# Optimization experiments

Measured on AMD Instinct MI355X. Metric: run time of the kernel, lower is better.

## Reference

```python
import jax, jax.numpy as jnp
import numpy as np

EPS = 1e-4  # Performer FAVOR+ stabilizing epsilon


def softmax_kernel(data, projection, is_query):
    # data: [b,h,s,d]; projection: [d,m] (already scaled by 1/sqrt(m) as in
    # redraw_projection_matrix). Performer softmax random-feature map:
    #   phi(x) = exp(x_hat @ P - ||x_hat||^2/2 - stabilizer) + eps
    d = data.shape[-1]
    data_normalizer = d ** -0.25
    data_dash = jnp.einsum('bhsd,dm->bhsm', data_normalizer * data, projection)
    diag = (jnp.sum(data * data, axis=-1, keepdims=True) * 0.5) * (data_normalizer ** 2)
    if is_query:
        stab = jnp.max(data_dash, axis=-1, keepdims=True)          # per-query max
    else:
        stab = jnp.max(data_dash, axis=(-2, -1), keepdims=True)    # per-head global max
    return jnp.exp(data_dash - diag - stab) + EPS


def setup_inputs() -> dict:
    key = jax.random.key(0)
    kq, kk, kv, kp = jax.random.split(key, 4)
    B, H, S, D, M = 4, 16, 1024, 64, 64
    q = jax.random.normal(kq, (B, H, S, D), dtype=jnp.float32)
    k = jax.random.normal(kk, (B, H, S, D), dtype=jnp.float32)
    v = jax.random.normal(kv, (B, H, S, D), dtype=jnp.float32)
    # simplex random matrix approximated by gaussian; scaled by 1/sqrt(n_features)
    projection_matrix = jax.random.normal(kp, (D, M), dtype=jnp.float32) / jnp.sqrt(jnp.float32(M))
    return {"q": q, "k": k, "v": v, "projection_matrix": projection_matrix}


def reference(q, k, v, projection_matrix):
    qp = softmax_kernel(q, projection_matrix, is_query=True)   # [b,h,s,m]
    kp = softmax_kernel(k, projection_matrix, is_query=False)  # [b,h,s,m]
    # torch impl: s = qp @ kp^T; causal tril; row-normalize; o = p @ v
    s = jnp.einsum('bhsm,bhtm->bhst', qp, kp)                  # [b,h,s,s]
    s = jnp.tril(s)
    p = s / jnp.sum(s, axis=-1, keepdims=True)
    return jnp.einsum('bhst,bhtd->bhsd', p, v)
```

## Files before the change

### kernel.cpp

```cpp
#include <hip/hip_runtime.h>
#include <hip/hip_bf16.h>


#define NRM 0.35355339059327373f
#define EPSF 1e-4f

typedef __attribute__((ext_vector_type(8))) short short8;
typedef __attribute__((ext_vector_type(4))) float f32x4;
typedef __attribute__((ext_vector_type(4))) unsigned uint4v;
typedef unsigned short u16;

__device__ inline u16 f2bf(float f) {
    unsigned u = __float_as_uint(f);
    return (u16)((u + 0x7FFFu + ((u >> 16) & 1u)) >> 16);
}
__device__ inline unsigned cvtpk(float lo, float hi) {
    unsigned r; asm("v_cvt_pk_bf16_f32 %0, %1, %2" : "=v"(r) : "v"(lo), "v"(hi)); return r;
}

__global__ __launch_bounds__(256) void kmax(
    const float* __restrict__ k, const float* __restrict__ proj,
    float* __restrict__ pmax, u16* __restrict__ ptg)
{
    __shared__ u16 PT[64][72];
    __shared__ float red[4];
    const int tid = threadIdx.x, lane = tid & 63, wave = tid >> 6;
    const int l15 = lane & 15, lhi = lane >> 4;
    const int b = blockIdx.x;

    #pragma unroll
    for (int p = 0; p < 4; ++p) {
        int d = p * 16 + (tid >> 4);
        int m = (tid & 15) * 4;
        float4 pv = *(const float4*)(proj + d * 64 + m);
        PT[m + 0][d] = f2bf(pv.x);
        PT[m + 1][d] = f2bf(pv.y);
        PT[m + 2][d] = f2bf(pv.z);
        PT[m + 3][d] = f2bf(pv.w);
    }
    __syncthreads();

    if (b == 0) {
        const int m = tid >> 2, c0 = (tid & 3) * 16;
        short8 x0 = *(const short8*)&PT[m][c0];
        short8 x1 = *(const short8*)&PT[m][c0 + 8];
        *(short8*)(ptg + m * 64 + c0)     = x0;
        *(short8*)(ptg + m * 64 + c0 + 8) = x1;
    }

    float m2 = -INFINITY;
    for (int i = 0; i < 4; ++i) {
        const int strip = b * 16 + wave * 4 + i;
        const int row0  = strip * 16;
        const float* xs = k + (size_t)(row0 + l15) * 64 + lhi * 8;
        float4 f0 = *(const float4*)(xs);
        float4 f1 = *(const float4*)(xs + 4);
        float4 f2 = *(const float4*)(xs + 32);
        float4 f3 = *(const float4*)(xs + 36);

        short8 a0, a1;
        a0[0] = (short)f2bf(f0.x); a0[1] = (short)f2bf(f0.y);
        a0[2] = (short)f2bf(f0.z); a0[3] = (short)f2bf(f0.w);
        a0[4] = (short)f2bf(f1.x); a0[5] = (short)f2bf(f1.y);
        a0[6] = (short)f2bf(f1.z); a0[7] = (short)f2bf(f1.w);
        a1[0] = (short)f2bf(f2.x); a1[1] = (short)f2bf(f2.y);
        a1[2] = (short)f2bf(f2.z); a1[3] = (short)f2bf(f2.w);
        a1[4] = (short)f2bf(f3.x); a1[5] = (short)f2bf(f3.y);
        a1[6] = (short)f2bf(f3.z); a1[7] = (short)f2bf(f3.w);

        f32x4 c[4] = { {0,0,0,0}, {0,0,0,0}, {0,0,0,0}, {0,0,0,0} };
        #pragma unroll
        for (int ct = 0; ct < 4; ++ct) {
            short8 b0 = *(const short8*)&PT[ct * 16 + l15][lhi * 8];
            short8 b1 = *(const short8*)&PT[ct * 16 + l15][32 + lhi * 8];
            c[ct] = __builtin_amdgcn_mfma_f32_16x16x32_bf16(a0, b0, c[ct], 0, 0, 0);
            c[ct] = __builtin_amdgcn_mfma_f32_16x16x32_bf16(a1, b1, c[ct], 0, 0, 0);
        }
        #pragma unroll
        for (int ct = 0; ct < 4; ++ct) {
            m2 = fmaxf(m2, fmaxf(fmaxf(c[ct][0], c[ct][1]), fmaxf(c[ct][2], c[ct][3])));
        }
    }
    m2 = fmaxf(m2, __shfl_xor(m2, 1));
    m2 = fmaxf(m2, __shfl_xor(m2, 2));
    m2 = fmaxf(m2, __shfl_xor(m2, 4));
    m2 = fmaxf(m2, __shfl_xor(m2, 8));
    m2 = fmaxf(m2, __shfl_xor(m2, 16));
    m2 = fmaxf(m2, __shfl_xor(m2, 32));
    if (lane == 0) red[wave] = m2 * NRM;
    __syncthreads();
    if (tid == 0)
        pmax[b] = fmaxf(fmaxf(red[0], red[1]), fmaxf(red[2], red[3]));
}

__global__ __launch_bounds__(256) void prep(
    const float* __restrict__ q, const float* __restrict__ k,
    const float* __restrict__ v, const u16* __restrict__ ptg,
    const float* __restrict__ pmax,
    u16* __restrict__ qp, u16* __restrict__ kp, u16* __restrict__ vT)
{
    __shared__ u16 tile[64][72];
    const int tid = threadIdx.x, lane = tid & 63, wave = tid >> 6;
    const int l15 = lane & 15, lhi = lane >> 4;
    const int bid = blockIdx.x;

    if (bid >= 512) {
        const int vb = bid - 512;
        for (int i = 0; i < 4; ++i) {
            const int t = vb * 4 + i;
            const int bh = t >> 4, s0 = (t & 15) << 6;
            const float* src = v + ((size_t)bh * 1024 + s0) * 64;
            #pragma unroll
            for (int p = 0; p < 4; ++p) {
                int s = p * 16 + (tid >> 4);
                int d = (tid & 15) * 4;
                float4 val = *(const float4*)(src + s * 64 + d);
                tile[d + 0][s] = f2bf(val.x);
                tile[d + 1][s] = f2bf(val.y);
                tile[d + 2][s] = f2bf(val.z);
                tile[d + 3][s] = f2bf(val.w);
            }
            __syncthreads();
            u16* dst = vT + (size_t)bh * 65536 + s0;
            #pragma unroll
            for (int p = 0; p < 4; ++p) {
                int d = p * 16 + (tid >> 4);
                int s = (tid & 15) * 4;
                ushort4 o;
                o.x = tile[d][s]; o.y = tile[d][s + 1];
                o.z = tile[d][s + 2]; o.w = tile[d][s + 3];
                *(ushort4*)(dst + d * 1024 + s) = o;
            }
            __syncthreads();
        }
        return;
    }

    const bool isQ = bid < 256;
    const float* x = isQ ? q : k;
    const int bid2 = bid & 255;

    short8 bf0[4], bf1[4];
    #pragma unroll
    for (int ct = 0; ct < 4; ++ct) {
        const u16* pr = ptg + (ct * 16 + l15) * 64 + lhi * 8;
        bf0[ct] = *(const short8*)(pr);
        bf1[ct] = *(const short8*)(pr + 32);
    }

    float stab = 0.f;
    if (!isQ) {
        const int h = bid2 >> 2;
        const float* pb = pmax + h * 4;
        stab = fmaxf(fmaxf(pb[0], pb[1]), fmaxf(pb[2], pb[3]));
    }

    for (int i = 0; i < 4; ++i) {
        const int strip = bid2 * 16 + wave * 4 + i;
        const int row0  = strip * 16;

        const float* xs = x + (size_t)(row0 + l15) * 64 + lhi * 8;
        float4 f0 = *(const float4*)(xs);
        float4 f1 = *(const float4*)(xs + 4);
        float4 f2 = *(const float4*)(xs + 32);
        float4 f3 = *(const float4*)(xs + 36);

        short8 a0, a1;
        a0[0] = (short)f2bf(f0.x); a0[1] = (short)f2bf(f0.y);
        a0[2] = (short)f2bf(f0.z); a0[3] = (short)f2bf(f0.w);
        a0[4] = (short)f2bf(f1.x); a0[5] = (short)f2bf(f1.y);
        a0[6] = (short)f2bf(f1.z); a0[7] = (short)f2bf(f1.w);
        a1[0] = (short)f2bf(f2.x); a1[1] = (short)f2bf(f2.y);
        a1[2] = (short)f2bf(f2.z); a1[3] = (short)f2bf(f2.w);
        a1[4] = (short)f2bf(f3.x); a1[5] = (short)f2bf(f3.y);
        a1[6] = (short)f2bf(f3.z); a1[7] = (short)f2bf(f3.w);

        float ss = f0.x*f0.x + f0.y*f0.y + f0.z*f0.z + f0.w*f0.w
                 + f1.x*f1.x + f1.y*f1.y + f1.z*f1.z + f1.w*f1.w
                 + f2.x*f2.x + f2.y*f2.y + f2.z*f2.z + f2.w*f2.w
                 + f3.x*f3.x + f3.y*f3.y + f3.z*f3.z + f3.w*f3.w;
        ss += __shfl_xor(ss, 16);
        ss += __shfl_xor(ss, 32);

        f32x4 c[4] = { {0,0,0,0}, {0,0,0,0}, {0,0,0,0}, {0,0,0,0} };
        #pragma unroll
        for (int ct = 0; ct < 4; ++ct) {
            c[ct] = __builtin_amdgcn_mfma_f32_16x16x32_bf16(a0, bf0[ct], c[ct], 0, 0, 0);
            c[ct] = __builtin_amdgcn_mfma_f32_16x16x32_bf16(a1, bf1[ct], c[ct], 0, 0, 0);
        }

        float diag[4];
        #pragma unroll
        for (int r = 0; r < 4; ++r) diag[r] = __shfl(ss, lhi * 4 + r) * 0.0625f;

        if (isQ) {
            float mx[4];
            #pragma unroll
            for (int r = 0; r < 4; ++r)
                mx[r] = fmaxf(fmaxf(c[0][r], c[1][r]), fmaxf(c[2][r], c[3][r]));
            #pragma unroll
            for (int r = 0; r < 4; ++r) {
                float m = mx[r];
                m = fmaxf(m, __shfl_xor(m, 1));
                m = fmaxf(m, __shfl_xor(m, 2));
                m = fmaxf(m, __shfl_xor(m, 4));
                m = fmaxf(m, __shfl_xor(m, 8));
                mx[r] = m;
            }
            u16* op = qp + (size_t)row0 * 64;
            #pragma unroll
            for (int ct = 0; ct < 4; ++ct) {
                #pragma unroll
                for (int r = 0; r < 4; ++r) {
                    float val = __expf(c[ct][r] * NRM - diag[r] - mx[r] * NRM) + EPSF;
                    op[(lhi * 4 + r) * 64 + ct * 16 + l15] = f2bf(val);
                }
            }
        } else {
            u16* op = kp + (size_t)row0 * 64;
            #pragma unroll
            for (int ct = 0; ct < 4; ++ct) {
                #pragma unroll
                for (int r = 0; r < 4; ++r) {
                    float val = __expf(c[ct][r] * NRM - diag[r] - stab) + EPSF;
                    op[(lhi * 4 + r) * 64 + ct * 16 + l15] = f2bf(val);
                }
            }
        }
    }
}

__global__ __launch_bounds__(256, 2) void attn(
    const u16* __restrict__ qp, const u16* __restrict__ kp,
    const u16* __restrict__ vT, float* __restrict__ out)
{
    __shared__ char lds[2][16384];

    const int tid = threadIdx.x, lane = tid & 63, wave = tid >> 6;
    const int l15 = lane & 15, lhi = lane >> 4;
    const int x = blockIdx.x;
    const int h = (((x >> 6) << 3)) | (x & 7);
    const int j = (x >> 3) & 7;

    const u16* kph = kp + (size_t)h * 65536;
    const u16* vTh = vT + (size_t)h * 65536;

    const int rch = lane >> 3;
    const int cb  = (lane & 7) * 16;
    const bool isK = wave < 2;
    const int cbase = (wave & 1) * 4;
    const int gstride = isK ? 4096 : 64;

    int lo0, lo1, lo2, lo3;
    const u16 *go0, *go1, *go2, *go3;
    {
        #define STG(cc, LO, GO)                                                 \
        {   int i = cbase + cc; int row = 8 * i + rch;                          \
            int nib = (row & 3) | (((row >> 3) & 1) << 2);                      \
            LO = (isK ? 0 : 8192) + row * 128 + (cb ^ (nib << 4));              \
            GO = isK ? (kph + row * 64 + (cb >> 1))                             \
                     : (vTh + (size_t)row * 1024 + (cb >> 1)); }
        STG(0, lo0, go0) STG(1, lo1, go1) STG(2, lo2, go2) STG(3, lo3, go3)
        #undef STG
    }

    const int rowp = 8 * (l15 >> 2) + (l15 & 3);
    const int nk = (l15 & 3) | (((l15 >> 2) & 1) << 2);
    const int nv = (l15 & 3) | (((l15 >> 3) & 1) << 2);
    const int ok0 = rowp * 128 + ((16 * lhi) ^ (nk << 4));
    const int ok1 = rowp * 128 + ((64 + 16 * lhi) ^ (nk << 4));
    const int ov0 = 8192 + l15 * 128 + ((16 * lhi) ^ (nv << 4));
    const int ov1 = 8192 + l15 * 128 + ((64 + 16 * lhi) ^ (nv << 4));

    short8 ls0, ls1, ls2, ls3;

    auto stageLoad = [&](int kt) {
        ls0 = *(const short8*)(go0 + (size_t)kt * gstride);
        ls1 = *(const short8*)(go1 + (size_t)kt * gstride);
        ls2 = *(const short8*)(go2 + (size_t)kt * gstride);
        ls3 = *(const short8*)(go3 + (size_t)kt * gstride);
    };
    auto stageWrite = [&](char* B) {
        *(short8*)(B + lo0) = ls0;
        *(short8*)(B + lo1) = ls1;
        *(short8*)(B + lo2) = ls2;
        *(short8*)(B + lo3) = ls3;
    };

    auto runStrip = [&](int sigma, int T) {
        const u16* qpr = qp + ((size_t)h * 1024 + sigma * 16 + l15) * 64 + lhi * 8;
        short8 aq0 = *(const short8*)(qpr);
        short8 aq1 = *(const short8*)(qpr + 32);
        const int qrl = ((sigma & 3) << 4) + l15;

        f32x4 acc0 = {0,0,0,0}, acc1 = {0,0,0,0}, acc2 = {0,0,0,0}, acc3 = {0,0,0,0};
        float den = 0.f;

        stageLoad(0);
        stageWrite(lds[0]);
        __syncthreads();

        int cur = 0;
        for (int kt = 0; kt <= T; ++kt) {
            if (kt < T) stageLoad(kt + 1);

            const char* B = lds[cur];
            short8 k0 = *(const short8*)(B + ok0);
            short8 k1 = *(const short8*)(B + ok1);
            short8 k2 = *(const short8*)(B + ok0 + 512);
            short8 k3 = *(const short8*)(B + ok1 + 512);
            short8 k4 = *(const short8*)(B + ok0 + 4096);
            short8 k5 = *(const short8*)(B + ok1 + 4096);
            short8 k6 = *(const short8*)(B + ok0 + 4608);
            short8 k7 = *(const short8*)(B + ok1 + 4608);
            short8 v0 = *(const short8*)(B + ov0);
            short8 v1 = *(const short8*)(B + ov1);
            short8 v2 = *(const short8*)(B + ov0 + 2048);
            short8 v3 = *(const short8*)(B + ov1 + 2048);
            short8 v4 = *(const short8*)(B + ov0 + 4096);
            short8 v5 = *(const short8*)(B + ov1 + 4096);
            short8 v6 = *(const short8*)(B + ov0 + 6144);
            short8 v7 = *(const short8*)(B + ov1 + 6144);

            f32x4 s0 = {0,0,0,0}, s1 = {0,0,0,0}, s2 = {0,0,0,0}, s3 = {0,0,0,0};
            __builtin_amdgcn_s_setprio(1);
            s0 = __builtin_amdgcn_mfma_f32_16x16x32_bf16(k0, aq0, s0, 0, 0, 0);
            s0 = __builtin_amdgcn_mfma_f32_16x16x32_bf16(k1, aq1, s0, 0, 0, 0);
            s1 = __builtin_amdgcn_mfma_f32_16x16x32_bf16(k2, aq0, s1, 0, 0, 0);
            s1 = __builtin_amdgcn_mfma_f32_16x16x32_bf16(k3, aq1, s1, 0, 0, 0);
            s2 = __builtin_amdgcn_mfma_f32_16x16x32_bf16(k4, aq0, s2, 0, 0, 0);
            s2 = __builtin_amdgcn_mfma_f32_16x16x32_bf16(k5, aq1, s2, 0, 0, 0);
            s3 = __builtin_amdgcn_mfma_f32_16x16x32_bf16(k6, aq0, s3, 0, 0, 0);
            s3 = __builtin_amdgcn_mfma_f32_16x16x32_bf16(k7, aq1, s3, 0, 0, 0);
            __builtin_amdgcn_s_setprio(0);

            if (kt == T) {
                const int kc = 8 * lhi;
                #pragma unroll
                for (int r = 0; r < 4; ++r) {
                    if (kc + r      > qrl) s0[r] = 0.f;
                    if (kc + 4 + r  > qrl) s1[r] = 0.f;
                    if (kc + 32 + r > qrl) s2[r] = 0.f;
                    if (kc + 36 + r > qrl) s3[r] = 0.f;
                }
            }
            float t0 = (s0[0] + s0[1]) + (s0[2] + s0[3]);
            float t1 = (s1[0] + s1[1]) + (s1[2] + s1[3]);
            float t2 = (s2[0] + s2[1]) + (s2[2] + s2[3]);
            float t3 = (s3[0] + s3[1]) + (s3[2] + s3[3]);
            den += (t0 + t1) + (t2 + t3);

            uint4v w0 = { cvtpk(s0[0], s0[1]), cvtpk(s0[2], s0[3]),
                          cvtpk(s1[0], s1[1]), cvtpk(s1[2], s1[3]) };
            uint4v w1 = { cvtpk(s2[0], s2[1]), cvtpk(s2[2], s2[3]),
                          cvtpk(s3[0], s3[1]), cvtpk(s3[2], s3[3]) };
            short8 pa0 = __builtin_bit_cast(short8, w0);
            short8 pa1 = __builtin_bit_cast(short8, w1);

            __builtin_amdgcn_s_setprio(1);
            acc0 = __builtin_amdgcn_mfma_f32_16x16x32_bf16(pa0, v0, acc0, 0, 0, 0);
            acc0 = __builtin_amdgcn_mfma_f32_16x16x32_bf16(pa1, v1, acc0, 0, 0, 0);
            acc1 = __builtin_amdgcn_mfma_f32_16x16x32_bf16(pa0, v2, acc1, 0, 0, 0);
            acc1 = __builtin_amdgcn_mfma_f32_16x16x32_bf16(pa1, v3, acc1, 0, 0, 0);
            acc2 = __builtin_amdgcn_mfma_f32_16x16x32_bf16(pa0, v4, acc2, 0, 0, 0);
            acc2 = __builtin_amdgcn_mfma_f32_16x16x32_bf16(pa1, v5, acc2, 0, 0, 0);
            acc3 = __builtin_amdgcn_mfma_f32_16x16x32_bf16(pa0, v6, acc3, 0, 0, 0);
            acc3 = __builtin_amdgcn_mfma_f32_16x16x32_bf16(pa1, v7, acc3, 0, 0, 0);
            __builtin_amdgcn_s_setprio(0);

            if (kt < T) stageWrite(lds[cur ^ 1]);
            __syncthreads();
            cur ^= 1;
        }

        den += __shfl_xor(den, 16);
        den += __shfl_xor(den, 32);
        float inv[4];
        #pragma unroll
        for (int r = 0; r < 4; ++r) inv[r] = 1.0f / __shfl(den, lhi * 4 + r);

        float* ob = out + ((size_t)h * 1024 + sigma * 16) * 64;
        #pragma unroll
        for (int r = 0; r < 4; ++r) {
            ob[(lhi * 4 + r) * 64 +  0 + l15] = acc0[r] * inv[r];
            ob[(lhi * 4 + r) * 64 + 16 + l15] = acc1[r] * inv[r];
            ob[(lhi * 4 + r) * 64 + 32 + l15] = acc2[r] * inv[r];
            ob[(lhi * 4 + r) * 64 + 48 + l15] = acc3[r] * inv[r];
        }
    };

    const int s0v = 4 * j + wave;
    runStrip(s0v, j);
    runStrip(63 - s0v, 15 - j);
}

extern "C" void kernel_launch(void* const* d_in, const int* in_sizes, int n_in,
                              void* d_out, int out_size, void* d_ws, size_t ws_size,
                              hipStream_t stream)
{
    const float* q    = (const float*)d_in[0];
    const float* k    = (const float*)d_in[1];
    const float* v    = (const float*)d_in[2];
    const float* proj = (const float*)d_in[3];
    float* out = (float*)d_out;

    char* ws = (char*)d_ws;
    u16*   qpw  = (u16*)(ws);
    u16*   kpw  = (u16*)(ws + (size_t)8 * 1024 * 1024);
    u16*   vTw  = (u16*)(ws + (size_t)16 * 1024 * 1024);
    float* pmax = (float*)(ws + (size_t)24 * 1024 * 1024);
    u16*   ptg  = (u16*)(ws + (size_t)24 * 1024 * 1024 + 4096);

    hipLaunchKernelGGL(kmax, dim3(256), dim3(256), 0, stream, k, proj, pmax, ptg);
    hipLaunchKernelGGL(prep, dim3(768), dim3(256), 0, stream,
                       q, k, v, ptg, pmax, qpw, kpw, vTw);
    hipLaunchKernelGGL(attn, dim3(512), dim3(256), 0, stream, qpw, kpw, vTw, out);
}
```

Before: 41.27 us.

## Fuse kmax, prep and attention into one cooperative kernel with grid syncs

Merges the three launches into a single cooperative kernel of 512 blocks. Each block computes its key strips' projections and keeps them in registers across a grid sync, so the key feature tensor is only written once after the global max is known and the key input is read once instead of twice. Query features and the V transpose are produced in the same phase, then a second grid sync precedes the causal attention loop. This removes launch gaps and redundant key loads, at the cost of two grid-wide barriers and a residency requirement of 2 blocks per CU. If the cooperative launch fails, it falls back to the old three-kernel path.

```diff
diff --git a/kernel.cpp b/kernel.cpp
--- a/kernel.cpp
+++ b/kernel.cpp
@@ -1,5 +1,8 @@
 #include <hip/hip_runtime.h>
 #include <hip/hip_bf16.h>
+#include <hip/hip_cooperative_groups.h>
+
+namespace cg = cooperative_groups;
 
 
 #define NRM 0.35355339059327373f
@@ -18,7 +21,375 @@
     unsigned r; asm("v_cvt_pk_bf16_f32 %0, %1, %2" : "=v"(r) : "v"(lo), "v"(hi)); return r;
 }
 
-__global__ __launch_bounds__(256) void kmax(
+__global__ __launch_bounds__(256, 2) void fused(
+    const float* __restrict__ q, const float* __restrict__ k,
+    const float* __restrict__ v, const float* __restrict__ proj,
+    float* __restrict__ pmax,
+    u16* __restrict__ qp, u16* __restrict__ kp, u16* __restrict__ vT,
+    float* __restrict__ out)
+{
+    __shared__ union {
+        struct { u16 PT[64][72]; u16 tile[64][72]; float red[4]; } p;
+        char attn[2][16384];
+    } smem;
+
+    const int tid = threadIdx.x, lane = tid & 63, wave = tid >> 6;
+    const int l15 = lane & 15, lhi = lane >> 4;
+    const int b = blockIdx.x;
+    cg::grid_group grid = cg::this_grid();
+
+    #pragma unroll
+    for (int p = 0; p < 4; ++p) {
+        int d = p * 16 + (tid >> 4);
+        int m = (tid & 15) * 4;
+        float4 pv = *(const float4*)(proj + d * 64 + m);
+        smem.p.PT[m + 0][d] = f2bf(pv.x);
+        smem.p.PT[m + 1][d] = f2bf(pv.y);
+        smem.p.PT[m + 2][d] = f2bf(pv.z);
+        smem.p.PT[m + 3][d] = f2bf(pv.w);
+    }
+    __syncthreads();
+
+    const int sA = b * 8 + wave * 2;
+    const int sB = sA + 1;
+
+    f32x4 cA[4] = {{0,0,0,0},{0,0,0,0},{0,0,0,0},{0,0,0,0}};
+    f32x4 cB[4] = {{0,0,0,0},{0,0,0,0},{0,0,0,0},{0,0,0,0}};
+    float diagA[4], diagB[4];
+    float m2 = -INFINITY;
+
+#define KSTRIP(SS, CC, DD)                                                      \
+    {                                                                           \
+        const int row0 = (SS) * 16;                                             \
+        const float* xs = k + (size_t)(row0 + l15) * 64 + lhi * 8;              \
+        float4 f0 = *(const float4*)(xs);                                       \
+        float4 f1 = *(const float4*)(xs + 4);                                   \
+        float4 f2 = *(const float4*)(xs + 32);                                  \
+        float4 f3 = *(const float4*)(xs + 36);                                  \
+        short8 a0, a1;                                                          \
+        a0[0]=(short)f2bf(f0.x); a0[1]=(short)f2bf(f0.y);                       \
+        a0[2]=(short)f2bf(f0.z); a0[3]=(short)f2bf(f0.w);                       \
+        a0[4]=(short)f2bf(f1.x); a0[5]=(short)f2bf(f1.y);                       \
+        a0[6]=(short)f2bf(f1.z); a0[7]=(short)f2bf(f1.w);                       \
+        a1[0]=(short)f2bf(f2.x); a1[1]=(short)f2bf(f2.y);                       \
+        a1[2]=(short)f2bf(f2.z); a1[3]=(short)f2bf(f2.w);                       \
+        a1[4]=(short)f2bf(f3.x); a1[5]=(short)f2bf(f3.y);                       \
+        a1[6]=(short)f2bf(f3.z); a1[7]=(short)f2bf(f3.w);                       \
+        float ss = f0.x*f0.x + f0.y*f0.y + f0.z*f0.z + f0.w*f0.w                \
+                 + f1.x*f1.x + f1.y*f1.y + f1.z*f1.z + f1.w*f1.w                \
+                 + f2.x*f2.x + f2.y*f2.y + f2.z*f2.z + f2.w*f2.w                \
+                 + f3.x*f3.x + f3.y*f3.y + f3.z*f3.z + f3.w*f3.w;               \
+        ss += __shfl_xor(ss, 16);                                               \
+        ss += __shfl_xor(ss, 32);                                               \
+        _Pragma("unroll")                                                       \
+        for (int ct = 0; ct < 4; ++ct) {                                        \
+            short8 b0 = *(const short8*)&smem.p.PT[ct*16 + l15][lhi*8];         \
+            short8 b1 = *(const short8*)&smem.p.PT[ct*16 + l15][32 + lhi*8];    \
+            CC[ct] = __builtin_amdgcn_mfma_f32_16x16x32_bf16(a0, b0, CC[ct],0,0,0); \
+            CC[ct] = __builtin_amdgcn_mfma_f32_16x16x32_bf16(a1, b1, CC[ct],0,0,0); \
+        }                                                                       \
+        _Pragma("unroll")                                                       \
+        for (int r = 0; r < 4; ++r) DD[r] = __shfl(ss, lhi * 4 + r) * 0.0625f;  \
+        _Pragma("unroll")                                                       \
+        for (int ct = 0; ct < 4; ++ct)                                          \
+            m2 = fmaxf(m2, fmaxf(fmaxf(CC[ct][0], CC[ct][1]),                   \
+                                 fmaxf(CC[ct][2], CC[ct][3])));                 \
+    }
+    KSTRIP(sA, cA, diagA)
+    KSTRIP(sB, cB, diagB)
+#undef KSTRIP
+
+    m2 = fmaxf(m2, __shfl_xor(m2, 1));
+    m2 = fmaxf(m2, __shfl_xor(m2, 2));
+    m2 = fmaxf(m2, __shfl_xor(m2, 4));
+    m2 = fmaxf(m2, __shfl_xor(m2, 8));
+    m2 = fmaxf(m2, __shfl_xor(m2, 16));
+    m2 = fmaxf(m2, __shfl_xor(m2, 32));
+    if (lane == 0) smem.p.red[wave] = m2 * NRM;
+
+    for (int i = 0; i < 2; ++i) {
+        const int strip = sA + i;
+        const int row0  = strip * 16;
+        const float* xs = q + (size_t)(row0 + l15) * 64 + lhi * 8;
+        float4 f0 = *(const float4*)(xs);
+        float4 f1 = *(const float4*)(xs + 4);
+        float4 f2 = *(const float4*)(xs + 32);
+        float4 f3 = *(const float4*)(xs + 36);
+
+        short8 a0, a1;
+        a0[0] = (short)f2bf(f0.x); a0[1] = (short)f2bf(f0.y);
+        a0[2] = (short)f2bf(f0.z); a0[3] = (short)f2bf(f0.w);
+        a0[4] = (short)f2bf(f1.x); a0[5] = (short)f2bf(f1.y);
+        a0[6] = (short)f2bf(f1.z); a0[7] = (short)f2bf(f1.w);
+        a1[0] = (short)f2bf(f2.x); a1[1] = (short)f2bf(f2.y);
+        a1[2] = (short)f2bf(f2.z); a1[3] = (short)f2bf(f2.w);
+        a1[4] = (short)f2bf(f3.x); a1[5] = (short)f2bf(f3.y);
+        a1[6] = (short)f2bf(f3.z); a1[7] = (short)f2bf(f3.w);
+
+        float ss = f0.x*f0.x + f0.y*f0.y + f0.z*f0.z + f0.w*f0.w
+                 + f1.x*f1.x + f1.y*f1.y + f1.z*f1.z + f1.w*f1.w
+                 + f2.x*f2.x + f2.y*f2.y + f2.z*f2.z + f2.w*f2.w
+                 + f3.x*f3.x + f3.y*f3.y + f3.z*f3.z + f3.w*f3.w;
+        ss += __shfl_xor(ss, 16);
+        ss += __shfl_xor(ss, 32);
+
+        f32x4 c[4] = { {0,0,0,0}, {0,0,0,0}, {0,0,0,0}, {0,0,0,0} };
+        #pragma unroll
+        for (int ct = 0; ct < 4; ++ct) {
+            short8 b0 = *(const short8*)&smem.p.PT[ct * 16 + l15][lhi * 8];
+            short8 b1 = *(const short8*)&smem.p.PT[ct * 16 + l15][32 + lhi * 8];
+            c[ct] = __builtin_amdgcn_mfma_f32_16x16x32_bf16(a0, b0, c[ct], 0, 0, 0);
+            c[ct] = __builtin_amdgcn_mfma_f32_16x16x32_bf16(a1, b1, c[ct], 0, 0, 0);
+        }
+
+        float diag[4];
+        #pragma unroll
+        for (int r = 0; r < 4; ++r) diag[r] = __shfl(ss, lhi * 4 + r) * 0.0625f;
+
+        float mx[4];
+        #pragma unroll
+        for (int r = 0; r < 4; ++r)
+            mx[r] = fmaxf(fmaxf(c[0][r], c[1][r]), fmaxf(c[2][r], c[3][r]));
+        #pragma unroll
+        for (int r = 0; r < 4; ++r) {
+            float m = mx[r];
+            m = fmaxf(m, __shfl_xor(m, 1));
+            m = fmaxf(m, __shfl_xor(m, 2));
+            m = fmaxf(m, __shfl_xor(m, 4));
+            m = fmaxf(m, __shfl_xor(m, 8));
+            mx[r] = m;
+        }
+        u16* op = qp + (size_t)row0 * 64;
+        #pragma unroll
+        for (int ct = 0; ct < 4; ++ct) {
+            #pragma unroll
+            for (int r = 0; r < 4; ++r) {
+                float val = __expf(c[ct][r] * NRM - diag[r] - mx[r] * NRM) + EPSF;
+                op[(lhi * 4 + r) * 64 + ct * 16 + l15] = f2bf(val);
+            }
+        }
+    }
+
+    __syncthreads();
+    if (tid == 0)
+        pmax[b] = fmaxf(fmaxf(smem.p.red[0], smem.p.red[1]),
+                        fmaxf(smem.p.red[2], smem.p.red[3]));
+
+    for (int i = 0; i < 2; ++i) {
+        const int t = b * 2 + i;
+        const int bh = t >> 4, s0 = (t & 15) << 6;
+        const float* src = v + ((size_t)bh * 1024 + s0) * 64;
+        #pragma unroll
+        for (int p = 0; p < 4; ++p) {
+            int s = p * 16 + (tid >> 4);
+            int d = (tid & 15) * 4;
+            float4 val = *(const float4*)(src + s * 64 + d);
+            smem.p.tile[d + 0][s] = f2bf(val.x);
+            smem.p.tile[d + 1][s] = f2bf(val.y);
+            smem.p.tile[d + 2][s] = f2bf(val.z);
+            smem.p.tile[d + 3][s] = f2bf(val.w);
+        }
+        __syncthreads();
+        u16* dst = vT + (size_t)bh * 65536 + s0;
+        #pragma unroll
+        for (int p = 0; p < 4; ++p) {
+            int d = p * 16 + (tid >> 4);
+            int s = (tid & 15) * 4;
+            ushort4 o;
+            o.x = smem.p.tile[d][s];     o.y = smem.p.tile[d][s + 1];
+            o.z = smem.p.tile[d][s + 2]; o.w = smem.p.tile[d][s + 3];
+            *(ushort4*)(dst + d * 1024 + s) = o;
+        }
+        __syncthreads();
+    }
+
+    grid.sync();
+
+    {
+        const int hb = b >> 3;
+        const float* pb = pmax + hb * 8;
+        float stab = fmaxf(fmaxf(fmaxf(pb[0], pb[1]), fmaxf(pb[2], pb[3])),
+                           fmaxf(fmaxf(pb[4], pb[5]), fmaxf(pb[6], pb[7])));
+#define KPOUT(SS, CC, DD)                                                       \
+        {                                                                       \
+            u16* op = kp + (size_t)((SS) * 16) * 64;                            \
+            _Pragma("unroll")                                                   \
+            for (int ct = 0; ct < 4; ++ct) {                                    \
+                _Pragma("unroll")                                               \
+                for (int r = 0; r < 4; ++r) {                                   \
+                    float val = __expf(CC[ct][r] * NRM - DD[r] - stab) + EPSF;  \
+                    op[(lhi * 4 + r) * 64 + ct * 16 + l15] = f2bf(val);         \
+                }                                                               \
+            }                                                                   \
+        }
+        KPOUT(sA, cA, diagA)
+        KPOUT(sB, cB, diagB)
+#undef KPOUT
+    }
+
+    grid.sync();
+
+    {
+    char (*lds)[16384] = smem.attn;
+
+    const int x = blockIdx.x;
+    const int h = (((x >> 6) << 3)) | (x & 7);
+    const int j = (x >> 3) & 7;
+
+    const u16* kph = kp + (size_t)h * 65536;
+    const u16* vTh = vT + (size_t)h * 65536;
+
+    const int rch = lane >> 3;
+    const int cb  = (lane & 7) * 16;
+    const bool isK = wave < 2;
+    const int cbase = (wave & 1) * 4;
+    const int gstride = isK ? 4096 : 64;
+
+    int lo0, lo1, lo2, lo3;
+    const u16 *go0, *go1, *go2, *go3;
+    {
+        #define STG(cc, LO, GO)                                                 \
+        {   int i = cbase + cc; int row = 8 * i + rch;                          \
+            int nib = (row & 3) | (((row >> 3) & 1) << 2);                      \
+            LO = (isK ? 0 : 8192) + row * 128 + (cb ^ (nib << 4));              \
+            GO = isK ? (kph + row * 64 + (cb >> 1))                             \
+                     : (vTh + (size_t)row * 1024 + (cb >> 1)); }
+        STG(0, lo0, go0) STG(1, lo1, go1) STG(2, lo2, go2) STG(3, lo3, go3)
+        #undef STG
+    }
+
+    const int rowp = 8 * (l15 >> 2) + (l15 & 3);
+    const int nk = (l15 & 3) | (((l15 >> 2) & 1) << 2);
+    const int nv = (l15 & 3) | (((l15 >> 3) & 1) << 2);
+    const int ok0 = rowp * 128 + ((16 * lhi) ^ (nk << 4));
+    const int ok1 = rowp * 128 + ((64 + 16 * lhi) ^ (nk << 4));
+    const int ov0 = 8192 + l15 * 128 + ((16 * lhi) ^ (nv << 4));
+    const int ov1 = 8192 + l15 * 128 + ((64 + 16 * lhi) ^ (nv << 4));
+
+    short8 ls0, ls1, ls2, ls3;
+
+    auto stageLoad = [&](int kt) {
+        ls0 = *(const short8*)(go0 + (size_t)kt * gstride);
+        ls1 = *(const short8*)(go1 + (size_t)kt * gstride);
+        ls2 = *(const short8*)(go2 + (size_t)kt * gstride);
+        ls3 = *(const short8*)(go3 + (size_t)kt * gstride);
+    };
+    auto stageWrite = [&](char* B) {
+        *(short8*)(B + lo0) = ls0;
+        *(short8*)(B + lo1) = ls1;
+        *(short8*)(B + lo2) = ls2;
+        *(short8*)(B + lo3) = ls3;
+    };
+
+    auto runStrip = [&](int sigma, int T) {
+        const u16* qpr = qp + ((size_t)h * 1024 + sigma * 16 + l15) * 64 + lhi * 8;
+        short8 aq0 = *(const short8*)(qpr);
+        short8 aq1 = *(const short8*)(qpr + 32);
+        const int qrl = ((sigma & 3) << 4) + l15;
+
+        f32x4 acc0 = {0,0,0,0}, acc1 = {0,0,0,0}, acc2 = {0,0,0,0}, acc3 = {0,0,0,0};
+        float den = 0.f;
+
+        stageLoad(0);
+        stageWrite(lds[0]);
+        __syncthreads();
+
+        int cur = 0;
+        for (int kt = 0; kt <= T; ++kt) {
+            if (kt < T) stageLoad(kt + 1);
+
+            const char* B = lds[cur];
+            short8 k0 = *(const short8*)(B + ok0);
+            short8 k1 = *(const short8*)(B + ok1);
+            short8 k2 = *(const short8*)(B + ok0 + 512);
+            short8 k3 = *(const short8*)(B + ok1 + 512);
+            short8 k4 = *(const short8*)(B + ok0 + 4096);
+            short8 k5 = *(const short8*)(B + ok1 + 4096);
+            short8 k6 = *(const short8*)(B + ok0 + 4608);
+            short8 k7 = *(const short8*)(B + ok1 + 4608);
+            short8 v0 = *(const short8*)(B + ov0);
+            short8 v1 = *(const short8*)(B + ov1);
+            short8 v2 = *(const short8*)(B + ov0 + 2048);
+            short8 v3 = *(const short8*)(B + ov1 + 2048);
+            short8 v4 = *(const short8*)(B + ov0 + 4096);
+            short8 v5 = *(const short8*)(B + ov1 + 4096);
+            short8 v6 = *(const short8*)(B + ov0 + 6144);
+            short8 v7 = *(const short8*)(B + ov1 + 6144);
+
+            f32x4 s0 = {0,0,0,0}, s1 = {0,0,0,0}, s2 = {0,0,0,0}, s3 = {0,0,0,0};
+            __builtin_amdgcn_s_setprio(1);
+            s0 = __builtin_amdgcn_mfma_f32_16x16x32_bf16(k0, aq0, s0, 0, 0, 0);
+            s0 = __builtin_amdgcn_mfma_f32_16x16x32_bf16(k1, aq1, s0, 0, 0, 0);
+            s1 = __builtin_amdgcn_mfma_f32_16x16x32_bf16(k2, aq0, s1, 0, 0, 0);
+            s1 = __builtin_amdgcn_mfma_f32_16x16x32_bf16(k3, aq1, s1, 0, 0, 0);
+            s2 = __builtin_amdgcn_mfma_f32_16x16x32_bf16(k4, aq0, s2, 0, 0, 0);
+            s2 = __builtin_amdgcn_mfma_f32_16x16x32_bf16(k5, aq1, s2, 0, 0, 0);
+            s3 = __builtin_amdgcn_mfma_f32_16x16x32_bf16(k6, aq0, s3, 0, 0, 0);
+            s3 = __builtin_amdgcn_mfma_f32_16x16x32_bf16(k7, aq1, s3, 0, 0, 0);
+            __builtin_amdgcn_s_setprio(0);
+
+            if (kt == T) {
+                const int kc = 8 * lhi;
+                #pragma unroll
+                for (int r = 0; r < 4; ++r) {
+                    if (kc + r      > qrl) s0[r] = 0.f;
+                    if (kc + 4 + r  > qrl) s1[r] = 0.f;
+                    if (kc + 32 + r > qrl) s2[r] = 0.f;
+                    if (kc + 36 + r > qrl) s3[r] = 0.f;
+                }
+            }
+            float t0 = (s0[0] + s0[1]) + (s0[2] + s0[3]);
+            float t1 = (s1[0] + s1[1]) + (s1[2] + s1[3]);
+            float t2 = (s2[0] + s2[1]) + (s2[2] + s2[3]);
+            float t3 = (s3[0] + s3[1]) + (s3[2] + s3[3]);
+            den += (t0 + t1) + (t2 + t3);
+
+            uint4v w0 = { cvtpk(s0[0], s0[1]), cvtpk(s0[2], s0[3]),
+                          cvtpk(s1[0], s1[1]), cvtpk(s1[2], s1[3]) };
+            uint4v w1 = { cvtpk(s2[0], s2[1]), cvtpk(s2[2], s2[3]),
+                          cvtpk(s3[0], s3[1]), cvtpk(s3[2], s3[3]) };
+            short8 pa0 = __builtin_bit_cast(short8, w0);
+            short8 pa1 = __builtin_bit_cast(short8, w1);
+
+            __builtin_amdgcn_s_setprio(1);
+            acc0 = __builtin_amdgcn_mfma_f32_16x16x32_bf16(pa0, v0, acc0, 0, 0, 0);
+            acc0 = __builtin_amdgcn_mfma_f32_16x16x32_bf16(pa1, v1, acc0, 0, 0, 0);
+            acc1 = __builtin_amdgcn_mfma_f32_16x16x32_bf16(pa0, v2, acc1, 0, 0, 0);
+            acc1 = __builtin_amdgcn_mfma_f32_16x16x32_bf16(pa1, v3, acc1, 0, 0, 0);
+            acc2 = __builtin_amdgcn_mfma_f32_16x16x32_bf16(pa0, v4, acc2, 0, 0, 0);
+            acc2 = __builtin_amdgcn_mfma_f32_16x16x32_bf16(pa1, v5, acc2, 0, 0, 0);
+            acc3 = __builtin_amdgcn_mfma_f32_16x16x32_bf16(pa0, v6, acc3, 0, 0, 0);
+            acc3 = __builtin_amdgcn_mfma_f32_16x16x32_bf16(pa1, v7, acc3, 0, 0, 0);
+            __builtin_amdgcn_s_setprio(0);
+
+            if (kt < T) stageWrite(lds[cur ^ 1]);
+            __syncthreads();
+            cur ^= 1;
+        }
+
+        den += __shfl_xor(den, 16);
+        den += __shfl_xor(den, 32);
+        float inv[4];
+        #pragma unroll
+        for (int r = 0; r < 4; ++r) inv[r] = 1.0f / __shfl(den, lhi * 4 + r);
+
+        float* ob = out + ((size_t)h * 1024 + sigma * 16) * 64;
+        #pragma unroll
+        for (int r = 0; r < 4; ++r) {
+            ob[(lhi * 4 + r) * 64 +  0 + l15] = acc0[r] * inv[r];
+            ob[(lhi * 4 + r) * 64 + 16 + l15] = acc1[r] * inv[r];
+            ob[(lhi * 4 + r) * 64 + 32 + l15] = acc2[r] * inv[r];
+            ob[(lhi * 4 + r) * 64 + 48 + l15] = acc3[r] * inv[r];
+        }
+    };
+
+    const int s0v = 4 * j + wave;
+    runStrip(s0v, j);
+    runStrip(63 - s0v, 15 - j);
+    }
+}
+
+__global__ __launch_bounds__(256) void kmax9(
     const float* __restrict__ k, const float* __restrict__ proj,
     float* __restrict__ pmax, u16* __restrict__ ptg)
 {
@@ -93,7 +464,7 @@
         pmax[b] = fmaxf(fmaxf(red[0], red[1]), fmaxf(red[2], red[3]));
 }
 
-__global__ __launch_bounds__(256) void prep(
+__global__ __launch_bounds__(256) void prep9(
     const float* __restrict__ q, const float* __restrict__ k,
     const float* __restrict__ v, const u16* __restrict__ ptg,
     const float* __restrict__ pmax,
@@ -230,7 +601,7 @@
     }
 }
 
-__global__ __launch_bounds__(256, 2) void attn(
+__global__ __launch_bounds__(256, 2) void attn9(
     const u16* __restrict__ qp, const u16* __restrict__ kp,
     const u16* __restrict__ vT, float* __restrict__ out)
 {
@@ -411,8 +782,14 @@
     float* pmax = (float*)(ws + (size_t)24 * 1024 * 1024);
     u16*   ptg  = (u16*)(ws + (size_t)24 * 1024 * 1024 + 4096);
 
-    hipLaunchKernelGGL(kmax, dim3(256), dim3(256), 0, stream, k, proj, pmax, ptg);
-    hipLaunchKernelGGL(prep, dim3(768), dim3(256), 0, stream,
-                       q, k, v, ptg, pmax, qpw, kpw, vTw);
-    hipLaunchKernelGGL(attn, dim3(512), dim3(256), 0, stream, qpw, kpw, vTw, out);
+    void* args[] = { (void*)&q, (void*)&k, (void*)&v, (void*)&proj,
+                     (void*)&pmax, (void*)&qpw, (void*)&kpw, (void*)&vTw, (void*)&out };
+    hipError_t err = hipLaunchCooperativeKernel((const void*)fused, dim3(512), dim3(256),
+                                                args, 0, stream);
+    if (err != hipSuccess) {
+        hipLaunchKernelGGL(kmax9, dim3(256), dim3(256), 0, stream, k, proj, pmax, ptg);
+        hipLaunchKernelGGL(prep9, dim3(768), dim3(256), 0, stream,
+                           q, k, v, ptg, pmax, qpw, kpw, vTw);
+        hipLaunchKernelGGL(attn9, dim3(512), dim3(256), 0, stream, qpw, kpw, vTw, out);
+    }
 }
```

Result: slower. 156.8 us (+279.9%).
